# Kernel tuning notes

Hardware: AMD Instinct MI355X
Metric: run time of the kernel (lower is better)

## Reference

```python
import jax
import jax.numpy as jnp
import numpy as np
from jax import lax


def setup_inputs() -> dict:
    key = jax.random.key(0)
    k0, k1 = jax.random.split(key)
    B, C, H, W = 8, 256, 96, 96
    FM0 = jax.random.normal(k0, (B, C, H, W), dtype=jnp.float32)
    FM1 = jax.random.normal(k1, (B, C, H, W), dtype=jnp.float32)
    return {"FM0": FM0, "FM1": FM1, "d_max": 4, "stride": 1}


def pointwise_correlation(FM0, FM1, d_max, stride):
    """out[b,h,w,i,j] = sum_c FM0[b,c,h,w] * FM1[b,c,h+(i-d)*s, w+(j-d)*s],
    with zero padding outside FM1's spatial extent."""
    B, C, H, W = FM0.shape
    D = 2 * d_max + 1
    p = d_max * stride
    FM1p = jnp.pad(FM1, ((0, 0), (0, 0), (p, p), (p, p)))
    offs = jnp.arange(D, dtype=jnp.int32) * stride  # start offsets into padded map
    ys, xs = jnp.meshgrid(offs, offs, indexing="ij")
    offsets = jnp.stack([ys.ravel(), xs.ravel()], axis=-1)  # (D*D, 2)

    def step(carry, off):
        sl = lax.dynamic_slice(FM1p, (0, 0, off[0], off[1]), (B, C, H, W))
        corr = jnp.einsum("bchw,bchw->bhw", FM0, sl)
        return carry, corr

    _, out = lax.scan(step, None, offsets)  # (D*D, B, H, W)
    out = out.reshape(D, D, B, H, W).transpose(2, 3, 4, 0, 1)  # (B, H, W, D, D)
    return out


def reference(FM0, FM1, d_max, stride):
    return pointwise_correlation(FM0, FM1, d_max, stride)
```

## Files before the change

### kernel.cpp

```cpp
#include <hip/hip_runtime.h>

#define HH 96
#define WW 96
#define CC 256
#define PLANE (HH * WW)
#define PITCH 40
#define AROWS 144
#define BROWS 704
#define LDSN ((AROWS + BROWS) * PITCH)
#define NOUT 81

typedef __attribute__((ext_vector_type(4))) float f32x4;
typedef __attribute__((ext_vector_type(2))) unsigned int u32x2;
typedef __attribute__((ext_vector_type(8))) __bf16 bf16x8;

static __device__ __forceinline__ unsigned int pkbf(float x, float y) {
  unsigned int ux = __builtin_bit_cast(unsigned int, x) + 0x8000u;
  unsigned int uy = __builtin_bit_cast(unsigned int, y) + 0x8000u;
  return __builtin_amdgcn_perm(uy, ux, 0x07060302u);
}

#define BAR_LGKM() asm volatile("s_waitcnt lgkmcnt(0)\n\ts_barrier" ::: "memory")

__global__ __launch_bounds__(384, 2) void corr_kernel(
    const float* __restrict__ fm0, const float* __restrict__ fm1,
    float* __restrict__ out) {
  __shared__ __align__(16) unsigned short lds[2 * LDSN];

  const int tid = threadIdx.x;
  const int bid = blockIdx.x;
  const int b = bid & 7;
  const int q = bid >> 3;
  const int s = q & 1;
  const int h0 = 3 * (q >> 1);

  const int lane = tid & 63;
  const int wv = tid >> 6;
  const int mm = lane & 15;
  const int kg = lane >> 4;

  const size_t boff = (size_t)b * CC * PLANE;

  if (wv >= 3) {
    const int pt = tid - 192;
    const float* gptr[9];
    int gdst[9];
    bool gact[9], gok[9];
    #pragma unroll
    for (int j = 0; j < 9; ++j) {
      const int g = pt + 192 * j;
      gact[j] = (g < 1696);
      if (g < 288) {
        const int a = g / 96, r = g % 96;
        const int wq = r >> 3, cq = r & 7;
        const int wst = 48 * s + 4 * wq;
        gok[j] = gact[j];
        gdst[j] = (a * 48 + 4 * wq) * PITCH + 4 * cq;
        gptr[j] = fm0 + boff + (size_t)(4 * cq) * PLANE + (h0 + a) * WW + wst;
      } else {
        const int gb = g - 288;
        const int i = gb >> 7, r = gb & 127;
        const int wq = r >> 3, cq = r & 7;
        const int hb = h0 - 4 + i;
        const int wst = 48 * s - 8 + 4 * wq;
        const bool ok = (hb >= 0) && (hb < HH) && (wst >= 0) && (wst < WW);
        gok[j] = ok && gact[j];
        gdst[j] = (AROWS + i * 64 + 4 * wq) * PITCH + 4 * cq;
        gptr[j] = fm1 + boff + (size_t)(4 * cq) * PLANE +
                  (size_t)(ok ? hb : 0) * WW + (ok ? wst : 0);
      }
    }

    f32x4 pre[9][4];
    #pragma unroll
    for (int j = 0; j < 9; ++j)
      #pragma unroll
      for (int cc = 0; cc < 4; ++cc) pre[j][cc] = f32x4{0.f, 0.f, 0.f, 0.f};

    #pragma unroll
    for (int j = 0; j < 9; ++j)
      if (gok[j]) {
        #pragma unroll
        for (int cc = 0; cc < 4; ++cc)
          pre[j][cc] = *(const f32x4*)(gptr[j] + (size_t)cc * PLANE);
      }
    #pragma unroll
    for (int j = 0; j < 9; ++j)
      if (gact[j]) {
        #pragma unroll
        for (int dw = 0; dw < 4; ++dw) {
          u32x2 v;
          v.x = pkbf(pre[j][0][dw], pre[j][1][dw]);
          v.y = pkbf(pre[j][2][dw], pre[j][3][dw]);
          *(u32x2*)&lds[gdst[j] + dw * PITCH] = v;
        }
      }
    #pragma unroll
    for (int j = 0; j < 9; ++j)
      if (gok[j]) {
        #pragma unroll
        for (int cc = 0; cc < 4; ++cc)
          pre[j][cc] = *(const f32x4*)(gptr[j] + (size_t)(32) * PLANE +
                                       (size_t)cc * PLANE);
      }
    BAR_LGKM();

    #pragma unroll 1
    for (int ks = 0; ks < 8; ++ks) {
      if (ks < 7) {
        const int bo = ((ks + 1) & 1) * LDSN;
        #pragma unroll
        for (int j = 0; j < 9; ++j)
          if (gact[j]) {
            #pragma unroll
            for (int dw = 0; dw < 4; ++dw) {
              u32x2 v;
              v.x = pkbf(pre[j][0][dw], pre[j][1][dw]);
              v.y = pkbf(pre[j][2][dw], pre[j][3][dw]);
              *(u32x2*)&lds[bo + gdst[j] + dw * PITCH] = v;
            }
          }
      }
      if (ks < 6) {
        const size_t koff = (size_t)((ks + 2) * 32) * PLANE;
        #pragma unroll
        for (int j = 0; j < 9; ++j)
          if (gok[j]) {
            #pragma unroll
            for (int cc = 0; cc < 4; ++cc)
              pre[j][cc] = *(const f32x4*)(gptr[j] + koff + (size_t)cc * PLANE);
          }
      }
      BAR_LGKM();
    }
  } else {
    f32x4 acc[9][3][2];
    #pragma unroll
    for (int i = 0; i < 9; ++i)
      #pragma unroll
      for (int mt = 0; mt < 3; ++mt) {
        acc[i][mt][0] = f32x4{0.f, 0.f, 0.f, 0.f};
        acc[i][mt][1] = f32x4{0.f, 0.f, 0.f, 0.f};
      }
    const int abase = (wv * 48 + mm) * PITCH + kg * 8;
    const int bbase = (AROWS + mm) * PITCH + kg * 8;

    asm volatile("s_barrier" ::: "memory");

    #pragma unroll 1
    for (int ks = 0; ks < 8; ++ks) {
      const int bo = (ks & 1) * LDSN;
      bf16x8 af[3];
      #pragma unroll
      for (int mt = 0; mt < 3; ++mt)
        af[mt] = *(const bf16x8*)&lds[bo + abase + 16 * mt * PITCH];
      #pragma unroll
      for (int i = 0; i < 9; ++i) {
        const int bb = bo + bbase + (wv + i) * 64 * PITCH;
        bf16x8 b0 = *(const bf16x8*)&lds[bb];
        #pragma unroll
        for (int mt = 0; mt < 3; ++mt) {
          bf16x8 b1 = *(const bf16x8*)&lds[bb + 16 * (mt + 1) * PITCH];
          acc[i][mt][0] = __builtin_amdgcn_mfma_f32_16x16x32_bf16(af[mt], b0, acc[i][mt][0], 0, 0, 0);
          acc[i][mt][1] = __builtin_amdgcn_mfma_f32_16x16x32_bf16(af[mt], b1, acc[i][mt][1], 0, 0, 0);
          b0 = b1;
        }
      }
      BAR_LGKM();
    }

    float* outb = out + ((size_t)b * PLANE + (size_t)(h0 + wv) * WW) * NOUT;
    #pragma unroll
    for (int u = 0; u < 2; ++u)
      #pragma unroll
      for (int rg = 0; rg < 4; ++rg) {
        const int j = 16 * u + mm - 4 * kg - rg - 4;
        if ((unsigned)j < 9u) {
          #pragma unroll
          for (int i = 0; i < 9; ++i)
            #pragma unroll
            for (int mt = 0; mt < 3; ++mt) {
              const int w = 48 * s + 16 * mt + 4 * kg + rg;
              outb[(size_t)w * NOUT + i * 9 + j] = acc[i][mt][u][rg];
            }
        }
      }
  }
}

extern "C" void kernel_launch(void* const* d_in, const int* in_sizes, int n_in,
                              void* d_out, int out_size, void* d_ws, size_t ws_size,
                              hipStream_t stream) {
  const float* fm0 = (const float*)d_in[0];
  const float* fm1 = (const float*)d_in[1];
  float* out = (float*)d_out;
  corr_kernel<<<dim3(512), dim3(384), 0, stream>>>(fm0, fm1, out);
}
```

Baseline: 233.8 us.

## Replace producer/consumer warp specialization with uniform waves sharing loads and MFMA

All six waves now both stage global-to-LDS loads (5 groups per thread instead of 9 across 3 producer waves) and perform MFMAs. Work per output row is split between two waves by the u half of the 32-wide diagonal band. Each wave holds 27 accumulators instead of 54. This removes idle producer waves and lowers register pressure per wave. The cost is that each wave now serializes its own loads, conversions and matrix work instead of overlapping them across specialized waves, and the A fragments are loaded redundantly by both waves of a pair.

```diff
diff --git a/kernel.cpp b/kernel.cpp
--- a/kernel.cpp
+++ b/kernel.cpp
@@ -9,6 +9,8 @@
 #define BROWS 704
 #define LDSN ((AROWS + BROWS) * PITCH)
 #define NOUT 81
+#define NGRP 1696
+#define GPT 5
 
 typedef __attribute__((ext_vector_type(4))) float f32x4;
 typedef __attribute__((ext_vector_type(2))) unsigned int u32x2;
@@ -38,153 +40,139 @@
   const int wv = tid >> 6;
   const int mm = lane & 15;
   const int kg = lane >> 4;
+  const int a = wv >> 1;
+  const int u = wv & 1;
 
   const size_t boff = (size_t)b * CC * PLANE;
 
-  if (wv >= 3) {
-    const int pt = tid - 192;
-    const float* gptr[9];
-    int gdst[9];
-    bool gact[9], gok[9];
+  const float* gptr[GPT];
+  int gdst[GPT];
+  bool gact[GPT], gok[GPT];
+  #pragma unroll
+  for (int j = 0; j < GPT; ++j) {
+    const int g = tid + 384 * j;
+    gact[j] = (g < NGRP);
+    if (g < 288) {
+      const int ar = g / 96, r = g % 96;
+      const int wq = r >> 3, cq = r & 7;
+      const int wst = 48 * s + 4 * wq;
+      gok[j] = gact[j];
+      gdst[j] = (ar * 48 + 4 * wq) * PITCH + 4 * cq;
+      gptr[j] = fm0 + boff + (size_t)(4 * cq) * PLANE + (h0 + ar) * WW + wst;
+    } else {
+      const int gb = g - 288;
+      const int i = gb >> 7, r = gb & 127;
+      const int wq = r >> 3, cq = r & 7;
+      const int hb = h0 - 4 + i;
+      const int wst = 48 * s - 8 + 4 * wq;
+      const bool ok = (hb >= 0) && (hb < HH) && (wst >= 0) && (wst < WW);
+      gok[j] = ok && gact[j];
+      gdst[j] = (AROWS + i * 64 + 4 * wq) * PITCH + 4 * cq;
+      gptr[j] = fm1 + boff + (size_t)(4 * cq) * PLANE +
+                (size_t)(ok ? hb : 0) * WW + (ok ? wst : 0);
+    }
+  }
+
+  f32x4 pre[GPT][4];
+  #pragma unroll
+  for (int j = 0; j < GPT; ++j)
     #pragma unroll
-    for (int j = 0; j < 9; ++j) {
-      const int g = pt + 192 * j;
-      gact[j] = (g < 1696);
-      if (g < 288) {
-        const int a = g / 96, r = g % 96;
-        const int wq = r >> 3, cq = r & 7;
-        const int wst = 48 * s + 4 * wq;
-        gok[j] = gact[j];
-        gdst[j] = (a * 48 + 4 * wq) * PITCH + 4 * cq;
-        gptr[j] = fm0 + boff + (size_t)(4 * cq) * PLANE + (h0 + a) * WW + wst;
-      } else {
-        const int gb = g - 288;
-        const int i = gb >> 7, r = gb & 127;
-        const int wq = r >> 3, cq = r & 7;
-        const int hb = h0 - 4 + i;
-        const int wst = 48 * s - 8 + 4 * wq;
-        const bool ok = (hb >= 0) && (hb < HH) && (wst >= 0) && (wst < WW);
-        gok[j] = ok && gact[j];
-        gdst[j] = (AROWS + i * 64 + 4 * wq) * PITCH + 4 * cq;
-        gptr[j] = fm1 + boff + (size_t)(4 * cq) * PLANE +
-                  (size_t)(ok ? hb : 0) * WW + (ok ? wst : 0);
+    for (int cc = 0; cc < 4; ++cc) pre[j][cc] = f32x4{0.f, 0.f, 0.f, 0.f};
+
+  f32x4 acc[9][3];
+  #pragma unroll
+  for (int i = 0; i < 9; ++i)
+    #pragma unroll
+    for (int mt = 0; mt < 3; ++mt) acc[i][mt] = f32x4{0.f, 0.f, 0.f, 0.f};
+
+  const int abase = (a * 48 + mm) * PITCH + kg * 8;
+  const int bbase = (AROWS + mm) * PITCH + kg * 8;
+
+  #pragma unroll
+  for (int j = 0; j < GPT; ++j)
+    if (gok[j]) {
+      #pragma unroll
+      for (int cc = 0; cc < 4; ++cc)
+        pre[j][cc] = *(const f32x4*)(gptr[j] + (size_t)cc * PLANE);
+    }
+  #pragma unroll
+  for (int j = 0; j < GPT; ++j)
+    if (gact[j]) {
+      #pragma unroll
+      for (int dw = 0; dw < 4; ++dw) {
+        u32x2 v;
+        v.x = pkbf(pre[j][0][dw], pre[j][1][dw]);
+        v.y = pkbf(pre[j][2][dw], pre[j][3][dw]);
+        *(u32x2*)&lds[gdst[j] + dw * PITCH] = v;
       }
     }
+  #pragma unroll
+  for (int j = 0; j < GPT; ++j)
+    if (gok[j]) {
+      #pragma unroll
+      for (int cc = 0; cc < 4; ++cc)
+        pre[j][cc] = *(const f32x4*)(gptr[j] + (size_t)32 * PLANE +
+                                     (size_t)cc * PLANE);
+    }
+  BAR_LGKM();
 
-    f32x4 pre[9][4];
+  #pragma unroll 1
+  for (int ks = 0; ks < 8; ++ks) {
+    const int bo = (ks & 1) * LDSN;
+    bf16x8 af[3];
     #pragma unroll
-    for (int j = 0; j < 9; ++j)
-      #pragma unroll
-      for (int cc = 0; cc < 4; ++cc) pre[j][cc] = f32x4{0.f, 0.f, 0.f, 0.f};
-
+    for (int mt = 0; mt < 3; ++mt)
+      af[mt] = *(const bf16x8*)&lds[bo + abase + 16 * mt * PITCH];
     #pragma unroll
-    for (int j = 0; j < 9; ++j)
-      if (gok[j]) {
-        #pragma unroll
-        for (int cc = 0; cc < 4; ++cc)
-          pre[j][cc] = *(const f32x4*)(gptr[j] + (size_t)cc * PLANE);
-      }
-    #pragma unroll
-    for (int j = 0; j < 9; ++j)
-      if (gact[j]) {
-        #pragma unroll
-        for (int dw = 0; dw < 4; ++dw) {
-          u32x2 v;
-          v.x = pkbf(pre[j][0][dw], pre[j][1][dw]);
-          v.y = pkbf(pre[j][2][dw], pre[j][3][dw]);
-          *(u32x2*)&lds[gdst[j] + dw * PITCH] = v;
-        }
-      }
-    #pragma unroll
-    for (int j = 0; j < 9; ++j)
-      if (gok[j]) {
-        #pragma unroll
-        for (int cc = 0; cc < 4; ++cc)
-          pre[j][cc] = *(const f32x4*)(gptr[j] + (size_t)(32) * PLANE +
-                                       (size_t)cc * PLANE);
-      }
-    BAR_LGKM();
-
-    #pragma unroll 1
-    for (int ks = 0; ks < 8; ++ks) {
-      if (ks < 7) {
-        const int bo = ((ks + 1) & 1) * LDSN;
-        #pragma unroll
-        for (int j = 0; j < 9; ++j)
-          if (gact[j]) {
-            #pragma unroll
-            for (int dw = 0; dw < 4; ++dw) {
-              u32x2 v;
-              v.x = pkbf(pre[j][0][dw], pre[j][1][dw]);
-              v.y = pkbf(pre[j][2][dw], pre[j][3][dw]);
-              *(u32x2*)&lds[bo + gdst[j] + dw * PITCH] = v;
-            }
-          }
-      }
-      if (ks < 6) {
-        const size_t koff = (size_t)((ks + 2) * 32) * PLANE;
-        #pragma unroll
-        for (int j = 0; j < 9; ++j)
-          if (gok[j]) {
-            #pragma unroll
-            for (int cc = 0; cc < 4; ++cc)
-              pre[j][cc] = *(const f32x4*)(gptr[j] + koff + (size_t)cc * PLANE);
-          }
-      }
-      BAR_LGKM();
-    }
-  } else {
-    f32x4 acc[9][3][2];
-    #pragma unroll
-    for (int i = 0; i < 9; ++i)
+    for (int i = 0; i < 9; ++i) {
+      const int bb = bo + bbase + (a + i) * 64 * PITCH;
       #pragma unroll
       for (int mt = 0; mt < 3; ++mt) {
-        acc[i][mt][0] = f32x4{0.f, 0.f, 0.f, 0.f};
-        acc[i][mt][1] = f32x4{0.f, 0.f, 0.f, 0.f};
+        bf16x8 bt = *(const bf16x8*)&lds[bb + 16 * (mt + u) * PITCH];
+        acc[i][mt] = __builtin_amdgcn_mfma_f32_16x16x32_bf16(af[mt], bt,
+                                                             acc[i][mt], 0, 0, 0);
       }
-    const int abase = (wv * 48 + mm) * PITCH + kg * 8;
-    const int bbase = (AROWS + mm) * PITCH + kg * 8;
+    }
+    if (ks < 7) {
+      const int bn = ((ks + 1) & 1) * LDSN;
+      #pragma unroll
+      for (int j = 0; j < GPT; ++j)
+        if (gact[j]) {
+          #pragma unroll
+          for (int dw = 0; dw < 4; ++dw) {
+            u32x2 v;
+            v.x = pkbf(pre[j][0][dw], pre[j][1][dw]);
+            v.y = pkbf(pre[j][2][dw], pre[j][3][dw]);
+            *(u32x2*)&lds[bn + gdst[j] + dw * PITCH] = v;
+          }
+        }
+    }
+    if (ks < 6) {
+      const size_t koff = (size_t)((ks + 2) * 32) * PLANE;
+      #pragma unroll
+      for (int j = 0; j < GPT; ++j)
+        if (gok[j]) {
+          #pragma unroll
+          for (int cc = 0; cc < 4; ++cc)
+            pre[j][cc] = *(const f32x4*)(gptr[j] + koff + (size_t)cc * PLANE);
+        }
+    }
+    BAR_LGKM();
+  }
 
-    asm volatile("s_barrier" ::: "memory");
-
-    #pragma unroll 1
-    for (int ks = 0; ks < 8; ++ks) {
-      const int bo = (ks & 1) * LDSN;
-      bf16x8 af[3];
+  float* outb = out + ((size_t)b * PLANE + (size_t)(h0 + a) * WW) * NOUT;
+  #pragma unroll
+  for (int rg = 0; rg < 4; ++rg) {
+    const int j = 16 * u + mm - 4 * kg - rg - 4;
+    if ((unsigned)j < 9u) {
       #pragma unroll
-      for (int mt = 0; mt < 3; ++mt)
-        af[mt] = *(const bf16x8*)&lds[bo + abase + 16 * mt * PITCH];
-      #pragma unroll
-      for (int i = 0; i < 9; ++i) {
-        const int bb = bo + bbase + (wv + i) * 64 * PITCH;
-        bf16x8 b0 = *(const bf16x8*)&lds[bb];
+      for (int i = 0; i < 9; ++i)
         #pragma unroll
         for (int mt = 0; mt < 3; ++mt) {
-          bf16x8 b1 = *(const bf16x8*)&lds[bb + 16 * (mt + 1) * PITCH];
-          acc[i][mt][0] = __builtin_amdgcn_mfma_f32_16x16x32_bf16(af[mt], b0, acc[i][mt][0], 0, 0, 0);
-          acc[i][mt][1] = __builtin_amdgcn_mfma_f32_16x16x32_bf16(af[mt], b1, acc[i][mt][1], 0, 0, 0);
-          b0 = b1;
+          const int w = 48 * s + 16 * mt + 4 * kg + rg;
+          outb[(size_t)w * NOUT + i * 9 + j] = acc[i][mt][rg];
         }
-      }
-      BAR_LGKM();
     }
-
-    float* outb = out + ((size_t)b * PLANE + (size_t)(h0 + wv) * WW) * NOUT;
-    #pragma unroll
-    for (int u = 0; u < 2; ++u)
-      #pragma unroll
-      for (int rg = 0; rg < 4; ++rg) {
-        const int j = 16 * u + mm - 4 * kg - rg - 4;
-        if ((unsigned)j < 9u) {
-          #pragma unroll
-          for (int i = 0; i < 9; ++i)
-            #pragma unroll
-            for (int mt = 0; mt < 3; ++mt) {
-              const int w = 48 * s + 16 * mt + 4 * kg + rg;
-              outb[(size_t)w * NOUT + i * 9 + j] = acc[i][mt][u][rg];
-            }
-        }
-      }
   }
 }
 
```

Result: faster. 212.1 us (-9.3%).
